# Optimization experiments

Hardware: AMD Instinct MI355X
Metric: run time of the kernel (lower is better)

## Reference

```python
import jax, jax.numpy as jnp
import numpy as np
from jax import lax

BIT = 9
QMAX = float(2 ** (BIT - 1) - 1)  # 255 for 9-bit symmetric


def fake_quant(v):
    """Symmetric per-tensor 9-bit fake quantization with STE."""
    scale = jnp.max(jnp.abs(v)) / QMAX
    scale = jnp.where(scale > 0, scale, jnp.ones_like(scale))
    q = jnp.round(v / scale) * scale
    return v + lax.stop_gradient(q - v)


def qconv(x, w):
    xq = fake_quant(x)
    wq = fake_quant(w)
    return lax.conv_general_dilated(
        xq, wq, window_strides=(1, 1), padding='VALID',
        dimension_numbers=('NCHW', 'OIHW', 'NCHW'))


def qfc(x, w):
    # x: [B, Fin], w: [Fout, Fin]
    return jnp.einsum('bi,oi->bo', fake_quant(x), fake_quant(w))


def maxpool2(x):
    return lax.reduce_window(x, -jnp.inf, lax.max,
                             (1, 1, 2, 2), (1, 1, 2, 2), 'VALID')


def setup_inputs() -> dict:
    key = jax.random.key(0)
    ks = jax.random.split(key, 6)
    x = jax.random.uniform(ks[0], (4096, 3, 32, 32), dtype=jnp.float32)
    def winit(k, shape):
        fan_in = int(np.prod(shape[1:]))
        return jax.random.normal(k, shape, dtype=jnp.float32) / np.sqrt(fan_in)
    w1 = winit(ks[1], (6, 3, 5, 5))
    w2 = winit(ks[2], (16, 6, 5, 5))
    w3 = winit(ks[3], (120, 16, 5, 5))
    w4 = winit(ks[4], (84, 120))
    w5 = winit(ks[5], (10, 84))
    return {'x': x, 'w1': w1, 'w2': w2, 'w3': w3, 'w4': w4, 'w5': w5}


def reference(x, w1, w2, w3, w4, w5):
    h = maxpool2(jax.nn.relu(qconv(x, w1)))        # [B,6,14,14]
    h = maxpool2(jax.nn.relu(qconv(h, w2)))        # [B,16,5,5]
    h = jax.nn.relu(qconv(h, w3))                  # [B,120,1,1]
    h = h.reshape(h.shape[0], -1)                  # [B,120]
    h = jax.nn.relu(qfc(h, w4))                    # [B,84]
    return qfc(h, w5)                              # [B,10]
```

## Files before the change

kernel.cpp:

```cpp
#include <hip/hip_runtime.h>
#include <hip/hip_bf16.h>

#define QMAX 255.0f

typedef __attribute__((ext_vector_type(8))) short short8;
typedef __attribute__((ext_vector_type(4))) float f32x4;

#define OFF_BF1   16
#define OFF_BF2   2064
#define OFF_BF3   6160
#define OFF_BF4   32784
#define OFF_BF5   38928
#define OFF_H1    40960
#define OFF_H2    5545984
#define OFF_H3    40960
#define OFF_H4    532480

#define IMG1 3080
#define IMG2 1352

__device__ __forceinline__ float get_scale(const unsigned* slots, int i) {
    float amax = __uint_as_float(slots[i]);
    float s = amax / QMAX;
    if (!(s > 0.0f)) s = 1.0f;
    return s;
}
__device__ __forceinline__ unsigned f2bf(float f) { return __float_as_uint(f) >> 16; }

__device__ __forceinline__ void amax_slot(unsigned* p, float v) {
    atomicMax((int*)p, (int)__float_as_uint(v));
}

__device__ __forceinline__ float block_maxN(float v, float* red, int nw) {
    #pragma unroll
    for (int off = 32; off > 0; off >>= 1) v = fmaxf(v, __shfl_xor(v, off));
    if ((threadIdx.x & 63) == 0) red[threadIdx.x >> 6] = v;
    __syncthreads();
    float m = red[0];
    for (int i = 1; i < nw; i++) m = fmaxf(m, red[i]);
    return m;
}

__global__ __launch_bounds__(256) void k_absmax_all(
    const float4* __restrict__ x4,
    const float* __restrict__ w1, const float* __restrict__ w2,
    const float* __restrict__ w3, const float* __restrict__ w4,
    const float* __restrict__ w5, unsigned* __restrict__ slots)
{
    __shared__ float red[4];
    int b = blockIdx.x, tid = threadIdx.x;
    float m = 0.0f;
    int slot = -1;
    if (b < 2048) {
        slot = 0;
        for (int i = b * 256 + tid; i < 3145728; i += 2048 * 256) {
            float4 v = x4[i];
            m = fmaxf(m, fmaxf(fmaxf(fabsf(v.x), fabsf(v.y)), fmaxf(fabsf(v.z), fabsf(v.w))));
        }
    } else {
        int b2 = b - 2048;
        const float* w = nullptr; int n = 0, start = 0, stride = 256;
        if (b2 < 48)      { w = w3; n = 48000; start = b2 * 256;        stride = 48 * 256; slot = 7; }
        else if (b2 < 58) { w = w4; n = 10080; start = (b2 - 48) * 256; stride = 10 * 256; slot = 8; }
        else if (b2 == 58){ w = w2; n = 2400;  slot = 6; }
        else if (b2 == 59){ w = w1; n = 450;   slot = 5; }
        else if (b2 == 60){ w = w5; n = 840;   slot = 9; }
        if (slot >= 0)
            for (int i = start + tid; i < n; i += stride) m = fmaxf(m, fabsf(w[i]));
    }
    m = block_maxN(m, red, 4);
    if (tid == 0 && slot >= 0) amax_slot(&slots[slot], m);
}

__global__ __launch_bounds__(256) void k_bfrag(
    const float* __restrict__ w1, const float* __restrict__ w2,
    const float* __restrict__ w3, const float* __restrict__ w4,
    const float* __restrict__ w5, const unsigned* __restrict__ slots,
    unsigned short* __restrict__ bf1, unsigned short* __restrict__ bf2,
    unsigned short* __restrict__ bf3, unsigned short* __restrict__ bf4,
    unsigned short* __restrict__ bf5)
{
    int idx = blockIdx.x * 256 + threadIdx.x;
    if (idx < 4096) {
        int f = idx, e = f & 7, l = (f >> 3) & 63, s = (f >> 9) & 3, H = f >> 11;
        int n = l & 15, g = l >> 4, C = 4 * s + g;
        float v = 0.f;
        if (n < 12 && C < 15) {
            int o = n >> 2, dx = n & 3, kx = e - dx;
            if (kx >= 0 && kx <= 4) {
                int c = C / 5, ky = C % 5, oc = 3 * H + o;
                v = rintf(w1[((oc * 3 + c) * 5 + ky) * 5 + kx] / get_scale(slots, 5));
            }
        }
        bf1[f] = (unsigned short)f2bf(v);
    } else if (idx < 12288) {
        int f = idx - 4096, e = f & 7, l = (f >> 3) & 63, s = (f >> 9) & 7, H = f >> 12;
        int n = l & 15, g = l >> 4, C = 4 * s + g;
        float v = 0.f;
        if (C < 30) {
            int o = n >> 1, dx = n & 1, kx = e - dx;
            if (kx >= 0 && kx <= 4) {
                int c = C / 5, ky = C % 5, oc = 8 * H + o;
                v = rintf(w2[((oc * 6 + c) * 5 + ky) * 5 + kx] / get_scale(slots, 6));
            }
        }
        bf2[f] = (unsigned short)f2bf(v);
    } else if (idx < 65536) {
        int f = idx - 12288, e = f & 7, l = (f >> 3) & 63, r = f >> 9;
        int s = r % 13, Nt = r / 13;
        int oc = Nt * 16 + (l & 15), k = 32 * s + 8 * (l >> 4) + e;
        float v = 0.f;
        if (oc < 120 && k < 400) v = rintf(w3[oc * 400 + k] / get_scale(slots, 7));
        bf3[f] = (unsigned short)f2bf(v);
    } else if (idx < 77824) {
        int f = idx - 65536, e = f & 7, l = (f >> 3) & 63, r = f >> 9;
        int s = r & 3, Nt = r >> 2;
        int oc = Nt * 16 + (l & 15), k = 32 * s + 8 * (l >> 4) + e;
        float v = 0.f;
        if (oc < 84 && k < 120) v = rintf(w4[oc * 120 + k] / get_scale(slots, 8));
        bf4[f] = (unsigned short)f2bf(v);
    } else if (idx < 79360) {
        int f = idx - 77824, e = f & 7, l = (f >> 3) & 63, s = f >> 9;
        int oc = l & 15, k = 32 * s + 8 * (l >> 4) + e;
        float v = 0.f;
        if (oc < 10 && k < 84) v = rintf(w5[oc * 84 + k] / get_scale(slots, 9));
        bf5[f] = (unsigned short)f2bf(v);
    }
}

__global__ __launch_bounds__(512) void k_conv1(
    const float* __restrict__ x, const unsigned short* __restrict__ bf1,
    const unsigned* __restrict__ slots, unsigned* __restrict__ slot_out,
    float* __restrict__ h1)
{
    __shared__ unsigned short xs[8 * IMG1];
    __shared__ float red[8];
    int b0 = blockIdx.x * 8, tid = threadIdx.x;
    int lane = tid & 63, wid = tid >> 6;
    int il = lane & 15, g = lane >> 4;
    short8 Bf[2][4];
    #pragma unroll
    for (int H = 0; H < 2; H++)
        #pragma unroll
        for (int s = 0; s < 4; s++)
            Bf[H][s] = *(const short8*)(bf1 + ((H * 4 + s) * 64 + lane) * 8);
    float sx = get_scale(slots, 0);
    #pragma unroll
    for (int img = 0; img < 8; img++) {
        const float* xb = x + (long)(b0 + img) * 3072;
        for (int i = tid; i < 768; i += 512) {
            int c = i >> 8, rem = i & 255, yy = rem >> 3, c4 = (rem & 7) << 2;
            float4 v = *(const float4*)(xb + c * 1024 + yy * 32 + c4);
            uint2 pk;
            pk.x = f2bf(rintf(v.x / sx)) | (f2bf(rintf(v.y / sx)) << 16);
            pk.y = f2bf(rintf(v.z / sx)) | (f2bf(rintf(v.w / sx)) << 16);
            *(uint2*)&xs[img * IMG1 + c * 1024 + yy * 32 + c4] = pk;
        }
    }
    __syncthreads();
    float mscale = sx * get_scale(slots, 5);

    int abase[4];
    #pragma unroll
    for (int s = 0; s < 4; s++) {
        int C = 4 * s + g; if (C > 14) C = 14;
        abase[s] = (il >> 1) * IMG1 + (C / 5) * 1024 + (C % 5) * 32;
    }
    int half = il & 1;
    int n = il, o = n >> 2;
    bool doSt2 = ((n & 3) == 0) && (n < 12);
    float vmax = 0.f;
    for (int uu = wid; uu < 49; uu += 8) {
        int pbe = uu / 14, pye = uu - 14 * pbe;
        int po = uu + 49;
        int pbo = po / 14, pyo = po - 14 * pbo;
        int pb = half ? pbo : pbe;
        int py = half ? pyo : pye;
        f32x4 acc[2][2];
        #pragma unroll
        for (int H = 0; H < 2; H++)
            #pragma unroll
            for (int yo = 0; yo < 2; yo++) acc[H][yo] = (f32x4){0.f, 0.f, 0.f, 0.f};
        #pragma unroll
        for (int yo = 0; yo < 2; yo++) {
            int y = 2 * py + yo;
            #pragma unroll
            for (int s = 0; s < 4; s++) {
                int addr = abase[s] + y * 32 + 4 * pb;
                union { unsigned long long u[2]; short8 v; } tA;
                tA.u[0] = *(const unsigned long long*)(xs + addr);
                tA.u[1] = *(const unsigned long long*)(xs + addr + 4);
                acc[0][yo] = __builtin_amdgcn_mfma_f32_16x16x32_bf16(tA.v, Bf[0][s], acc[0][yo], 0, 0, 0);
                acc[1][yo] = __builtin_amdgcn_mfma_f32_16x16x32_bf16(tA.v, Bf[1][s], acc[1][yo], 0, 0, 0);
            }
        }
        #pragma unroll
        for (int H = 0; H < 2; H++)
            #pragma unroll
            for (int r = 0; r < 4; r++) {
                float m = fmaxf(acc[H][0][r], acc[H][1][r]);
                float pooled = fmaxf(m, __shfl_xor(m, 1));
                float partner = __shfl_xor(pooled, 2);
                if (doSt2) {
                    int imgr = 2 * g + (r >> 1);
                    int pbr = (r & 1) ? pbo : pbe;
                    int pyr = (r & 1) ? pyo : pye;
                    float v0 = fmaxf(pooled * mscale, 0.f);
                    float v1 = fmaxf(partner * mscale, 0.f);
                    int oc = 3 * H + o;
                    *(float2*)&h1[((long)(b0 + imgr) * 6 + oc) * 224 + pyr * 16 + 2 * pbr] =
                        make_float2(v0, v1);
                    vmax = fmaxf(vmax, fmaxf(v0, v1));
                }
            }
    }
    vmax = block_maxN(vmax, red, 8);
    if (tid == 0) amax_slot(slot_out, vmax);
}

__global__ __launch_bounds__(256) void k_conv2(
    const float* __restrict__ h1, const unsigned short* __restrict__ bf2,
    const unsigned* __restrict__ slots, unsigned* __restrict__ slot_out,
    float* __restrict__ h2)
{
    __shared__ unsigned short xs[4 * IMG2];
    __shared__ float red[4];
    int b0 = blockIdx.x * 4, tid = threadIdx.x;
    int lane = tid & 63, wid = tid >> 6;
    int il = lane & 15, g = lane >> 4;
    short8 Bf[2][8];
    #pragma unroll
    for (int H = 0; H < 2; H++)
        #pragma unroll
        for (int s = 0; s < 8; s++)
            Bf[H][s] = *(const short8*)(bf2 + ((H * 8 + s) * 64 + lane) * 8);
    float s1 = get_scale(slots, 1);
    #pragma unroll
    for (int img = 0; img < 4; img++) {
        const float4* src = (const float4*)(h1 + (long)(b0 + img) * 1344);
        for (int i = tid; i < 336; i += 256) {
            float4 v = src[i];
            unsigned pk0 = f2bf(rintf(v.x / s1)) | (f2bf(rintf(v.y / s1)) << 16);
            unsigned pk1 = f2bf(rintf(v.z / s1)) | (f2bf(rintf(v.w / s1)) << 16);
            *(uint2*)&xs[img * IMG2 + 4 * i] = make_uint2(pk0, pk1);
        }
    }
    __syncthreads();
    float mscale = s1 * get_scale(slots, 6);

    int abase[8];
    #pragma unroll
    for (int s = 0; s < 8; s++) {
        int C = 4 * s + g; if (C > 29) C = 29;
        abase[s] = (il >> 2) * IMG2 + (C / 5) * 224 + (C % 5) * 16;
    }
    int q = il & 3;
    int offq = (q == 0) ? 0 : (6 * q + 1);
    int n = il, o = n >> 1;
    bool doStCol = ((n & 1) == 0);
    float vmax = 0.f;
    for (int uu = wid; uu < 7; uu += 4) {
        int p = offq + uu; if (p > 24) p = 24;
        int pb = p / 5, py = p % 5;
        f32x4 acc[2][2];
        #pragma unroll
        for (int H = 0; H < 2; H++)
            #pragma unroll
            for (int yo = 0; yo < 2; yo++) acc[H][yo] = (f32x4){0.f, 0.f, 0.f, 0.f};
        #pragma unroll
        for (int yo = 0; yo < 2; yo++) {
            int y = 2 * py + yo;
            #pragma unroll
            for (int s = 0; s < 8; s++) {
                int addr = abase[s] + y * 16 + 2 * pb;
                union { unsigned u[4]; short8 v; } tA;
                tA.u[0] = *(const unsigned*)(xs + addr);
                tA.u[1] = *(const unsigned*)(xs + addr + 2);
                tA.u[2] = *(const unsigned*)(xs + addr + 4);
                tA.u[3] = *(const unsigned*)(xs + addr + 6);
                acc[0][yo] = __builtin_amdgcn_mfma_f32_16x16x32_bf16(tA.v, Bf[0][s], acc[0][yo], 0, 0, 0);
                acc[1][yo] = __builtin_amdgcn_mfma_f32_16x16x32_bf16(tA.v, Bf[1][s], acc[1][yo], 0, 0, 0);
            }
        }
        #pragma unroll
        for (int H = 0; H < 2; H++)
            #pragma unroll
            for (int r = 0; r < 4; r++) {
                float m = fmaxf(acc[H][0][r], acc[H][1][r]);
                float pooled = fmaxf(m, __shfl_xor(m, 1));
                int cntr = (r == 0) ? 7 : 6;
                if (doStCol && uu < cntr) {
                    int offr = (r == 0) ? 0 : (6 * r + 1);
                    int pr = offr + uu, pbr = pr / 5, pyr = pr % 5;
                    float v = fmaxf(pooled * mscale, 0.f);
                    int oc = 8 * H + o;
                    h2[((long)(b0 + g) * 16 + oc) * 25 + pyr * 5 + pbr] = v;
                    vmax = fmaxf(vmax, v);
                }
            }
    }
    vmax = block_maxN(vmax, red, 4);
    if (tid == 0) amax_slot(slot_out, vmax);
}

__global__ __launch_bounds__(512) void k_conv3(
    const float* __restrict__ h2, const unsigned short* __restrict__ bf3,
    const unsigned* __restrict__ slots, unsigned* __restrict__ slot_out,
    float* __restrict__ h3)
{
    __shared__ unsigned short xs[16 * 408];
    __shared__ float red[8];
    int b0 = blockIdx.x * 16, tid = threadIdx.x;
    int lane = tid & 63, wid = tid >> 6;
    int il = lane & 15, g = lane >> 4;
    short8 Bf[13];
    #pragma unroll
    for (int s = 0; s < 13; s++)
        Bf[s] = *(const short8*)(bf3 + ((wid * 13 + s) * 64 + lane) * 8);
    float s2 = get_scale(slots, 2);
    for (int i = tid; i < 3200; i += 512) {
        int img = i / 200, p = i % 200;
        float2 v = *(const float2*)(h2 + (long)(b0 + img) * 400 + 2 * p);
        unsigned pk = f2bf(rintf(v.x / s2)) | (f2bf(rintf(v.y / s2)) << 16);
        *(unsigned*)&xs[img * 408 + 2 * p] = pk;
    }
    __syncthreads();
    float mscale = s2 * get_scale(slots, 7);
    f32x4 acc = (f32x4){0.f, 0.f, 0.f, 0.f};
    #pragma unroll
    for (int s = 0; s < 13; s++) {
        int C = 4 * s + g; if (C > 49) C = 49;
        int addr = il * 408 + 8 * C;
        union { unsigned long long u[2]; short8 v; } tA;
        tA.u[0] = *(const unsigned long long*)(xs + addr);
        tA.u[1] = *(const unsigned long long*)(xs + addr + 4);
        acc = __builtin_amdgcn_mfma_f32_16x16x32_bf16(tA.v, Bf[s], acc, 0, 0, 0);
    }
    float vmax = 0.f;
    int oc = wid * 16 + il;
    if (oc < 120) {
        #pragma unroll
        for (int r = 0; r < 4; r++) {
            float v = fmaxf(acc[r] * mscale, 0.f);
            h3[(long)(b0 + 4 * g + r) * 120 + oc] = v;
            vmax = fmaxf(vmax, v);
        }
    }
    vmax = block_maxN(vmax, red, 8);
    if (tid == 0) amax_slot(slot_out, vmax);
}

__global__ __launch_bounds__(512) void k_fc4(
    const float* __restrict__ h3, const unsigned short* __restrict__ bf4,
    const unsigned* __restrict__ slots, unsigned* __restrict__ slot_out,
    float* __restrict__ h4)
{
    __shared__ unsigned short xs[16 * 136];
    __shared__ float red[8];
    int b0 = blockIdx.x * 16, tid = threadIdx.x;
    int lane = tid & 63, wid = tid >> 6;
    int il = lane & 15, g = lane >> 4;
    short8 Bf[4];
    if (wid < 6) {
        #pragma unroll
        for (int s = 0; s < 4; s++)
            Bf[s] = *(const short8*)(bf4 + ((wid * 4 + s) * 64 + lane) * 8);
    }
    float s3 = get_scale(slots, 3);
    for (int i = tid; i < 960; i += 512) {
        int img = i / 60, p = i % 60;
        float2 v = *(const float2*)(h3 + (long)(b0 + img) * 120 + 2 * p);
        unsigned pk = f2bf(rintf(v.x / s3)) | (f2bf(rintf(v.y / s3)) << 16);
        *(unsigned*)&xs[img * 136 + 2 * p] = pk;
    }
    __syncthreads();
    float mscale = s3 * get_scale(slots, 8);
    float vmax = 0.f;
    if (wid < 6) {
        f32x4 acc = (f32x4){0.f, 0.f, 0.f, 0.f};
        #pragma unroll
        for (int s = 0; s < 4; s++) {
            int C = 4 * s + g; if (C > 14) C = 14;
            int addr = il * 136 + 8 * C;
            union { unsigned long long u[2]; short8 v; } tA;
            tA.u[0] = *(const unsigned long long*)(xs + addr);
            tA.u[1] = *(const unsigned long long*)(xs + addr + 4);
            acc = __builtin_amdgcn_mfma_f32_16x16x32_bf16(tA.v, Bf[s], acc, 0, 0, 0);
        }
        int oc = wid * 16 + il;
        if (oc < 84) {
            #pragma unroll
            for (int r = 0; r < 4; r++) {
                float v = fmaxf(acc[r] * mscale, 0.f);
                h4[(long)(b0 + 4 * g + r) * 84 + oc] = v;
                vmax = fmaxf(vmax, v);
            }
        }
    }
    vmax = block_maxN(vmax, red, 8);
    if (tid == 0) amax_slot(slot_out, vmax);
}

__global__ __launch_bounds__(256) void k_fc5(
    const float* __restrict__ h4, const unsigned short* __restrict__ bf5,
    const unsigned* __restrict__ slots, float* __restrict__ out)
{
    __shared__ unsigned short xs[4 * 16 * 104];
    int tid = threadIdx.x;
    int lane = tid & 63, w = tid >> 6;
    int il = lane & 15, g = lane >> 4;
    int b0w = blockIdx.x * 64 + w * 16;
    short8 Bf[3];
    #pragma unroll
    for (int s = 0; s < 3; s++)
        Bf[s] = *(const short8*)(bf5 + ((s * 64) + lane) * 8);
    float s4 = get_scale(slots, 4);
    for (int i = lane; i < 672; i += 64) {
        int img = i / 42, j = i % 42;
        float2 v = *(const float2*)(h4 + (long)(b0w + img) * 84 + 2 * j);
        unsigned pk = f2bf(rintf(v.x / s4)) | (f2bf(rintf(v.y / s4)) << 16);
        *(unsigned*)&xs[w * 1664 + img * 104 + 2 * j] = pk;
    }
    for (int i = lane; i < 96; i += 64) {
        int img = i / 6, j = i % 6;
        *(unsigned*)&xs[w * 1664 + img * 104 + 84 + 2 * j] = 0u;
    }
    __syncthreads();
    float mscale = s4 * get_scale(slots, 9);
    f32x4 acc = (f32x4){0.f, 0.f, 0.f, 0.f};
    #pragma unroll
    for (int s = 0; s < 3; s++) {
        int addr = w * 1664 + il * 104 + 32 * s + 8 * g;
        union { unsigned long long u[2]; short8 v; } tA;
        tA.u[0] = *(const unsigned long long*)(xs + addr);
        tA.u[1] = *(const unsigned long long*)(xs + addr + 4);
        acc = __builtin_amdgcn_mfma_f32_16x16x32_bf16(tA.v, Bf[s], acc, 0, 0, 0);
    }
    if (il < 10) {
        #pragma unroll
        for (int r = 0; r < 4; r++)
            out[(long)(b0w + 4 * g + r) * 10 + il] = acc[r] * mscale;
    }
}

extern "C" void kernel_launch(void* const* d_in, const int* in_sizes, int n_in,
                              void* d_out, int out_size, void* d_ws, size_t ws_size,
                              hipStream_t stream) {
    const float* x  = (const float*)d_in[0];
    const float* w1 = (const float*)d_in[1];
    const float* w2 = (const float*)d_in[2];
    const float* w3 = (const float*)d_in[3];
    const float* w4 = (const float*)d_in[4];
    const float* w5 = (const float*)d_in[5];
    float* out = (float*)d_out;
    float* ws = (float*)d_ws;
    unsigned* slots = (unsigned*)d_ws;
    unsigned short* bf1 = (unsigned short*)(ws + OFF_BF1);
    unsigned short* bf2 = (unsigned short*)(ws + OFF_BF2);
    unsigned short* bf3 = (unsigned short*)(ws + OFF_BF3);
    unsigned short* bf4 = (unsigned short*)(ws + OFF_BF4);
    unsigned short* bf5 = (unsigned short*)(ws + OFF_BF5);
    float* h1 = ws + OFF_H1;
    float* h2 = ws + OFF_H2;
    float* h3 = ws + OFF_H3;
    float* h4 = ws + OFF_H4;

    k_absmax_all<<<2112, 256, 0, stream>>>((const float4*)x, w1, w2, w3, w4, w5, slots);
    k_bfrag<<<310, 256, 0, stream>>>(w1, w2, w3, w4, w5, slots, bf1, bf2, bf3, bf4, bf5);
    k_conv1<<<512, 512, 0, stream>>>(x, bf1, slots, slots + 1, h1);
    k_conv2<<<1024, 256, 0, stream>>>(h1, bf2, slots, slots + 2, h2);
    k_conv3<<<256, 512, 0, stream>>>(h2, bf3, slots, slots + 3, h3);
    k_fc4<<<256, 512, 0, stream>>>(h3, bf4, slots, slots + 4, h4);
    k_fc5<<<64, 256, 0, stream>>>(h4, bf5, slots, out);
}
```

Measured before the change: 109.1 us.

## Remap conv1 MFMA work so each wave owns a row and stores float4

Restructures conv1's output tiling. Each of 7 waves now handles one pooled row across all 7 column blocks, instead of 8 waves striding over 49 tiles. Lane halves are remapped to rows 7 apart through a 448-element offset, and pooled results from adjacent column blocks are paired so h1 is written with float4 stores instead of float2. This is meant to cut address arithmetic and the number of global store transactions. In exchange, one of the 8 waves sits idle, and padding zeros are written in the last column block.

```diff
diff --git a/kernel.cpp b/kernel.cpp
--- a/kernel.cpp
+++ b/kernel.cpp
@@ -164,55 +164,66 @@
     #pragma unroll
     for (int s = 0; s < 4; s++) {
         int C = 4 * s + g; if (C > 14) C = 14;
-        abase[s] = (il >> 1) * IMG1 + (C / 5) * 1024 + (C % 5) * 32;
-    }
-    int half = il & 1;
-    int n = il, o = n >> 2;
-    bool doSt2 = ((n & 3) == 0) && (n < 12);
+        abase[s] = (il >> 1) * IMG1 + (C / 5) * 1024 + (C % 5) * 32 + (il & 1) * 448;
+    }
+    int o = il >> 2;
+    bool doSt = ((il & 3) == 0) && (il < 12);
     float vmax = 0.f;
-    for (int uu = wid; uu < 49; uu += 8) {
-        int pbe = uu / 14, pye = uu - 14 * pbe;
-        int po = uu + 49;
-        int pbo = po / 14, pyo = po - 14 * pbo;
-        int pb = half ? pbo : pbe;
-        int py = half ? pyo : pye;
-        f32x4 acc[2][2];
-        #pragma unroll
-        for (int H = 0; H < 2; H++)
-            #pragma unroll
-            for (int yo = 0; yo < 2; yo++) acc[H][yo] = (f32x4){0.f, 0.f, 0.f, 0.f};
-        #pragma unroll
-        for (int yo = 0; yo < 2; yo++) {
-            int y = 2 * py + yo;
-            #pragma unroll
-            for (int s = 0; s < 4; s++) {
-                int addr = abase[s] + y * 32 + 4 * pb;
-                union { unsigned long long u[2]; short8 v; } tA;
-                tA.u[0] = *(const unsigned long long*)(xs + addr);
-                tA.u[1] = *(const unsigned long long*)(xs + addr + 4);
-                acc[0][yo] = __builtin_amdgcn_mfma_f32_16x16x32_bf16(tA.v, Bf[0][s], acc[0][yo], 0, 0, 0);
-                acc[1][yo] = __builtin_amdgcn_mfma_f32_16x16x32_bf16(tA.v, Bf[1][s], acc[1][yo], 0, 0, 0);
-            }
-        }
-        #pragma unroll
-        for (int H = 0; H < 2; H++)
-            #pragma unroll
-            for (int r = 0; r < 4; r++) {
-                float m = fmaxf(acc[H][0][r], acc[H][1][r]);
-                float pooled = fmaxf(m, __shfl_xor(m, 1));
-                float partner = __shfl_xor(pooled, 2);
-                if (doSt2) {
-                    int imgr = 2 * g + (r >> 1);
-                    int pbr = (r & 1) ? pbo : pbe;
-                    int pyr = (r & 1) ? pyo : pye;
-                    float v0 = fmaxf(pooled * mscale, 0.f);
-                    float v1 = fmaxf(partner * mscale, 0.f);
-                    int oc = 3 * H + o;
-                    *(float2*)&h1[((long)(b0 + imgr) * 6 + oc) * 224 + pyr * 16 + 2 * pbr] =
-                        make_float2(v0, v1);
-                    vmax = fmaxf(vmax, fmaxf(v0, v1));
+    if (wid < 7) {
+        int uu = wid;
+        int ybase = uu * 64;
+        f32x4 v0[2][2], v1[2][2];
+        #pragma unroll
+        for (int pb = 0; pb < 7; pb++) {
+            f32x4 acc[2][2];
+            #pragma unroll
+            for (int H = 0; H < 2; H++)
+                #pragma unroll
+                for (int yo = 0; yo < 2; yo++) acc[H][yo] = (f32x4){0.f, 0.f, 0.f, 0.f};
+            #pragma unroll
+            for (int yo = 0; yo < 2; yo++) {
+                #pragma unroll
+                for (int s = 0; s < 4; s++) {
+                    int addr = abase[s] + ybase + yo * 32 + 4 * pb;
+                    union { unsigned long long u[2]; short8 v; } tA;
+                    tA.u[0] = *(const unsigned long long*)(xs + addr);
+                    tA.u[1] = *(const unsigned long long*)(xs + addr + 4);
+                    acc[0][yo] = __builtin_amdgcn_mfma_f32_16x16x32_bf16(tA.v, Bf[0][s], acc[0][yo], 0, 0, 0);
+                    acc[1][yo] = __builtin_amdgcn_mfma_f32_16x16x32_bf16(tA.v, Bf[1][s], acc[1][yo], 0, 0, 0);
                 }
             }
+            #pragma unroll
+            for (int H = 0; H < 2; H++) {
+                #pragma unroll
+                for (int r = 0; r < 4; r++) {
+                    float ym = fmaxf(acc[H][0][r], acc[H][1][r]);
+                    float p  = fmaxf(ym, __shfl_xor(ym, 1));
+                    v0[H][pb & 1][r] = p;
+                    v1[H][pb & 1][r] = __shfl_xor(p, 2);
+                }
+            }
+            if ((pb & 1) || pb == 6) {
+                int pxb = (pb == 6) ? 12 : 2 * (pb - 1);
+                bool last = (pb == 6);
+                if (doSt) {
+                    #pragma unroll
+                    for (int H = 0; H < 2; H++)
+                        #pragma unroll
+                        for (int r = 0; r < 4; r++) {
+                            int imgr = 2 * g + (r >> 1);
+                            int pyr = 7 * (r & 1) + uu;
+                            int oc = 3 * H + o;
+                            float a0 = fmaxf(v0[H][0][r] * mscale, 0.f);
+                            float a1 = fmaxf(v1[H][0][r] * mscale, 0.f);
+                            float a2 = last ? 0.f : fmaxf(v0[H][1][r] * mscale, 0.f);
+                            float a3 = last ? 0.f : fmaxf(v1[H][1][r] * mscale, 0.f);
+                            *(float4*)&h1[((long)(b0 + imgr) * 6 + oc) * 224 + pyr * 16 + pxb] =
+                                make_float4(a0, a1, a2, a3);
+                            vmax = fmaxf(vmax, fmaxf(fmaxf(a0, a1), fmaxf(a2, a3)));
+                        }
+                }
+            }
+        }
     }
     vmax = block_maxN(vmax, red, 8);
     if (tid == 0) amax_slot(slot_out, vmax);
```

New measurement: 104.0 us, median of 3. -4.6%, faster.
